# Kernel tuning notes

Hardware: AMD Instinct MI355X
Metric: run time of the kernel (lower is better)

## Reference

```python
import jax, jax.numpy as jnp
import numpy as np

K = 161  # frequency bins
T = 2000  # time frames
M_INIT = 5.0  # initial triangular window width (args.m)


def setup_inputs() -> dict:
    key = jax.random.key(0)
    k1, k2 = jax.random.split(key)
    # learned window-width parameter, initialized near args.m with small jitter
    m = M_INIT + 0.5 * jax.random.normal(k1, (K, T, 1), dtype=jnp.float32)
    # spectrogram input, indexed as input[0, 0, :, :] in the original
    x = jax.random.normal(k2, (1, 1, K, T), dtype=jnp.float32)
    input_length = T
    return {"m": m, "x": x, "input_length": input_length}


def reference(m, x, input_length):
    # m: (K, T, 1) learned param; x: (1, 1, K, T) spectrogram.
    k = m.shape[0]
    am = jnp.abs(m)[:, :, 0]                      # (K, T)  == abs_m broadcast
    idx = jnp.arange(k, dtype=jnp.float32)
    # |range1 - range2|[i, t, j] = |j - i|, independent of t -> (K, K)
    d = jnp.abs(idx[None, :] - idx[:, None])      # d[i, j] = |j - i|
    wide = am > 1.0                               # (K, T) window-vs-delta mask
    # triangular window: relu(|m| - |j-i|) / m^2 (safe denom where branch unused)
    am2 = jnp.where(wide, am * am, 1.0)
    tri = jax.nn.relu(am[:, :, None] - d[:, None, :]) / am2[:, :, None]  # (K,T,K)
    delta = jnp.eye(k, dtype=jnp.float32)[:, None, :]                    # (i==j)
    blar = jnp.where(wide[:, :, None], tri, delta)                       # (K,T,K)
    blar = blar / jnp.sum(blar, axis=2, keepdims=True)                   # normalize over j
    # out[j, t] = sum_i blar[i, t, j] * x[i, t]
    xs = x[0, 0]                                  # (K, T)
    smoothed = jnp.einsum('itj,it->jt', blar, xs)  # (K, T)
    return smoothed.reshape(1, 1, k, xs.shape[1])
```

## Files before the change

### kernel.cpp

```cpp
#include <hip/hip_runtime.h>

#define KBINS 161
#define TFRAMES 2000

__global__ __launch_bounds__(256) void m_noise_smooth_kernel(
    const float* __restrict__ m,
    const float* __restrict__ x,
    float* __restrict__ out) {
  const int t = blockIdx.x;
  const int tid = threadIdx.x;

  __shared__ float s_am[KBINS];
  __shared__ float s_scale[KBINS];
  __shared__ float s_x[KBINS];
  __shared__ float s_red[256];

  float am = 0.0f;
  if (tid < KBINS) {
    const int i = tid;
    am = fabsf(m[i * TFRAMES + t]);
    s_am[i] = am;
    s_x[i] = x[i * TFRAMES + t];

    float S = am;
    int dmax = (int)am;
    if (dmax > KBINS - 1) dmax = KBINS - 1;
    for (int d = 1; d <= dmax; ++d) {
      int cnt = (i - d >= 0) + (i + d < KBINS);
      S += (am - (float)d) * (float)cnt;
    }
    const bool wide = am > 1.0f;
    s_scale[i] = wide ? (1.0f / S) : 0.0f;
  }

  s_red[tid] = am;
  __syncthreads();
  for (int s = 128; s > 0; s >>= 1) {
    if (tid < s) s_red[tid] = fmaxf(s_red[tid], s_red[tid + s]);
    __syncthreads();
  }
  const float maxam = s_red[0];

  if (tid < KBINS) {
    const int j = tid;
    int R = (int)ceilf(maxam);
    if (R > KBINS - 1) R = KBINS - 1;
    const int lo = (j - R > 0) ? (j - R) : 0;
    const int hi = (j + R < KBINS - 1) ? (j + R) : (KBINS - 1);

    float acc = (s_scale[j] == 0.0f) ? s_x[j] : 0.0f;

    for (int i = lo; i <= hi; ++i) {
      const float d = fabsf((float)(j - i));
      const float w = fmaxf(s_am[i] - d, 0.0f) * s_scale[i];
      acc = fmaf(w, s_x[i], acc);
    }
    out[j * TFRAMES + t] = acc;
  }
}

extern "C" void kernel_launch(void* const* d_in, const int* in_sizes, int n_in,
                              void* d_out, int out_size, void* d_ws, size_t ws_size,
                              hipStream_t stream) {
  const float* m = (const float*)d_in[0];
  const float* x = (const float*)d_in[1];
  float* out = (float*)d_out;

  m_noise_smooth_kernel<<<TFRAMES, 256, 0, stream>>>(m, x, out);
}
```

Baseline: 65.77 us.

## Tile eight time frames per block with float4 loads and wave-shuffle max

Each block now handles eight consecutive time frames instead of one. Inputs are loaded with float4 vector reads into a shared tile, and the max reduction uses wavefront shuffles instead of a shared-memory tree with many barriers. This aims to coalesce the strided column reads and to cut per-block launch and sync overhead. In exchange there are only 250 blocks, which may underfill the GPU, and the shared R is now the max over eight frames, so the inner loop can run longer.

```diff
diff --git a/kernel.cpp b/kernel.cpp
--- a/kernel.cpp
+++ b/kernel.cpp
@@ -2,60 +2,73 @@
 
 #define KBINS 161
 #define TFRAMES 2000
+#define TILE_T 8
 
 __global__ __launch_bounds__(256) void m_noise_smooth_kernel(
     const float* __restrict__ m,
     const float* __restrict__ x,
     float* __restrict__ out) {
-  const int t = blockIdx.x;
+  const int t0 = blockIdx.x * TILE_T;
   const int tid = threadIdx.x;
 
-  __shared__ float s_am[KBINS];
-  __shared__ float s_scale[KBINS];
-  __shared__ float s_x[KBINS];
-  __shared__ float s_red[256];
+  __shared__ float s_am[KBINS * TILE_T];
+  __shared__ float s_scale[KBINS * TILE_T];
+  __shared__ float s_x[KBINS * TILE_T];
+  __shared__ float s_wmax[4];
 
-  float am = 0.0f;
-  if (tid < KBINS) {
-    const int i = tid;
-    am = fabsf(m[i * TFRAMES + t]);
-    s_am[i] = am;
-    s_x[i] = x[i * TFRAMES + t];
+  float thread_max = 0.0f;
 
-    float S = am;
-    int dmax = (int)am;
-    if (dmax > KBINS - 1) dmax = KBINS - 1;
-    for (int d = 1; d <= dmax; ++d) {
-      int cnt = (i - d >= 0) + (i + d < KBINS);
-      S += (am - (float)d) * (float)cnt;
-    }
-    const bool wide = am > 1.0f;
-    s_scale[i] = wide ? (1.0f / S) : 0.0f;
+  for (int q = tid; q < KBINS * 2; q += 256) {
+    const int i = q >> 1;
+    const int h = (q & 1) * 4;
+    const float4 v = *(const float4*)(x + i * TFRAMES + t0 + h);
+    *(float4*)(s_x + i * TILE_T + h) = v;
   }
 
-  s_red[tid] = am;
+  for (int q = tid; q < KBINS * 2; q += 256) {
+    const int i = q >> 1;
+    const int h = (q & 1) * 4;
+    const float4 v = *(const float4*)(m + i * TFRAMES + t0 + h);
+    const float vv[4] = {v.x, v.y, v.z, v.w};
+#pragma unroll
+    for (int e = 0; e < 4; ++e) {
+      const float am = fabsf(vv[e]);
+      thread_max = fmaxf(thread_max, am);
+      float S = am;
+      int dmax = (int)am;
+      if (dmax > KBINS - 1) dmax = KBINS - 1;
+      for (int d = 1; d <= dmax; ++d) {
+        const int cnt = (i - d >= 0) + (i + d < KBINS);
+        S += (am - (float)d) * (float)cnt;
+      }
+      s_am[i * TILE_T + h + e] = am;
+      s_scale[i * TILE_T + h + e] = (am > 1.0f) ? (1.0f / S) : 0.0f;
+    }
+  }
+
+#pragma unroll
+  for (int off = 32; off > 0; off >>= 1)
+    thread_max = fmaxf(thread_max, __shfl_xor(thread_max, off, 64));
+  if ((tid & 63) == 0) s_wmax[tid >> 6] = thread_max;
   __syncthreads();
-  for (int s = 128; s > 0; s >>= 1) {
-    if (tid < s) s_red[tid] = fmaxf(s_red[tid], s_red[tid + s]);
-    __syncthreads();
-  }
-  const float maxam = s_red[0];
+  const float maxam =
+      fmaxf(fmaxf(s_wmax[0], s_wmax[1]), fmaxf(s_wmax[2], s_wmax[3]));
+  int R = (int)ceilf(maxam);
+  if (R > KBINS - 1) R = KBINS - 1;
 
-  if (tid < KBINS) {
-    const int j = tid;
-    int R = (int)ceilf(maxam);
-    if (R > KBINS - 1) R = KBINS - 1;
+  const int t_ = tid & 7;
+  for (int j = (tid >> 3); j < KBINS; j += 32) {
     const int lo = (j - R > 0) ? (j - R) : 0;
     const int hi = (j + R < KBINS - 1) ? (j + R) : (KBINS - 1);
-
-    float acc = (s_scale[j] == 0.0f) ? s_x[j] : 0.0f;
-
+    const float sc_j = s_scale[j * TILE_T + t_];
+    float acc = (sc_j == 0.0f) ? s_x[j * TILE_T + t_] : 0.0f;
     for (int i = lo; i <= hi; ++i) {
-      const float d = fabsf((float)(j - i));
-      const float w = fmaxf(s_am[i] - d, 0.0f) * s_scale[i];
-      acc = fmaf(w, s_x[i], acc);
+      const float w =
+          fmaxf(s_am[i * TILE_T + t_] - fabsf((float)(j - i)), 0.0f) *
+          s_scale[i * TILE_T + t_];
+      acc = fmaf(w, s_x[i * TILE_T + t_], acc);
     }
-    out[j * TFRAMES + t] = acc;
+    out[j * TFRAMES + t0 + t_] = acc;
   }
 }
 
@@ -66,5 +79,5 @@
   const float* x = (const float*)d_in[1];
   float* out = (float*)d_out;
 
-  m_noise_smooth_kernel<<<TFRAMES, 256, 0, stream>>>(m, x, out);
+  m_noise_smooth_kernel<<<TFRAMES / TILE_T, 256, 0, stream>>>(m, x, out);
 }
```

Result: slower. 68.28 us (+3.8%).
